# Performance work log

Hardware: AMD Instinct MI355X
Metric: run time of the kernel (lower is better)

The kernel has to match this reference:

```python
import jax, jax.numpy as jnp
import numpy as np

D_MODEL = 1024
NUM_HEADS = 16
HEAD_DIM = D_MODEL // NUM_HEADS
WINDOW = 64
GLOBAL_TOKENS = 4
MAX_SEQ_LEN = 2048
RANDOM_TOKENS = 32
BATCH = 2
SEQ = 2048
NEG = -1.0e9
LN_EPS = 1e-5


def setup_inputs() -> dict:
    key = jax.random.key(0)
    k1, k2, k3, k4 = jax.random.split(key, 4)
    x = jax.random.normal(k1, (BATCH, SEQ, D_MODEL), dtype=jnp.float32)
    w_qkv = jax.random.normal(k2, (D_MODEL, 3 * D_MODEL), dtype=jnp.float32) * (D_MODEL ** -0.5)
    w_out = jax.random.normal(k3, (D_MODEL, D_MODEL), dtype=jnp.float32) * (D_MODEL ** -0.5)
    ln_gamma = jnp.ones((D_MODEL,), dtype=jnp.float32)
    ln_beta = jnp.zeros((D_MODEL,), dtype=jnp.float32)
    rand_idx = jax.random.randint(k4, (MAX_SEQ_LEN, RANDOM_TOKENS), 0, MAX_SEQ_LEN, dtype=jnp.int32)
    return {"x": x, "w_qkv": w_qkv, "w_out": w_out,
            "ln_gamma": ln_gamma, "ln_beta": ln_beta, "rand_idx": rand_idx}


def _build_masks(seq_len, rand_idx):
    i = jnp.arange(seq_len)
    causal = (i[:, None] >= i[None, :]).astype(jnp.float32)  # [L,L], lower-triangular
    # local window mask
    dist = jnp.abs(i[:, None] - i[None, :])
    local = (dist <= WINDOW).astype(jnp.float32) * causal
    # global column mask: columns {0..G-1} u {L-G..L-1}, rows i >= g (== causal on those cols)
    gcols = jnp.concatenate([jnp.arange(GLOBAL_TOKENS), jnp.arange(seq_len - GLOBAL_TOKENS, seq_len)])
    is_gcol = jnp.zeros((seq_len,), jnp.float32).at[gcols].set(1.0)
    glob = is_gcol[None, :] * causal
    # random mask: per-row fixed random columns, then causal-filtered
    ri = rand_idx[:seq_len]  # [L, R]
    rows = jnp.broadcast_to(i[:, None], ri.shape)
    rnd = jnp.zeros((seq_len, seq_len), jnp.float32).at[rows, ri].set(1.0) * causal
    return local, glob, rnd


def reference(x, w_qkv, w_out, ln_gamma, ln_beta, rand_idx):
    B, L, _ = x.shape
    residual = x
    # LayerNorm
    mu = jnp.mean(x, axis=-1, keepdims=True)
    var = jnp.mean(jnp.square(x - mu), axis=-1, keepdims=True)
    xn = (x - mu) * jax.lax.rsqrt(var + LN_EPS) * ln_gamma + ln_beta
    # QKV projection
    qkv = xn @ w_qkv
    q, k, v = jnp.split(qkv, 3, axis=-1)
    q = q.reshape(B, L, NUM_HEADS, HEAD_DIM).transpose(0, 2, 1, 3)  # [B,H,L,D]
    k = k.reshape(B, L, NUM_HEADS, HEAD_DIM).transpose(0, 2, 1, 3)
    v = v.reshape(B, L, NUM_HEADS, HEAD_DIM).transpose(0, 2, 1, 3)
    local, glob, rnd = _build_masks(L, rand_idx)
    raw = jnp.einsum('bhqd,bhkd->bhqk', q, k) / jnp.sqrt(jnp.float32(HEAD_DIM))
    # original sums three masked copies of the same scores:
    # combined = 3*raw + ((1-local)+(1-glob)+(1-rnd)) * NEG
    penalty = (3.0 - (local + glob + rnd)) * NEG  # [L,L]
    combined = 3.0 * raw + penalty[None, None, :, :]
    attn = jax.nn.softmax(combined, axis=-1)
    out = jnp.einsum('bhqk,bhkd->bhqd', attn, v)
    out = out.transpose(0, 2, 1, 3).reshape(B, L, D_MODEL)
    out = out @ w_out
    return out + residual
```

## Files before the change

kernel.cpp:

```cpp
#include <hip/hip_runtime.h>
#include <stdint.h>

typedef __attribute__((ext_vector_type(8))) short shortx8;
typedef __attribute__((ext_vector_type(4))) float floatx4;

static constexpr int SEQ_    = 2048;
static constexpr int DMODEL  = 1024;
static constexpr int HDIM    = 64;
static constexpr int BATCH_  = 2;
static constexpr int NHEADS  = 16;
static constexpr int WINDOW_ = 64;
static constexpr int GTOK    = 4;
static constexpr int RTOK    = 32;
static constexpr int ROWS    = BATCH_ * SEQ_;
static constexpr int QKVN    = 3 * DMODEL;

__device__ inline unsigned short f2bf(float f) {
  union { float f; unsigned int u; } x; x.f = f;
  unsigned int r = (x.u + 0x7FFFu + ((x.u >> 16) & 1u)) >> 16;
  return (unsigned short)r;
}
__device__ inline float bf2f(unsigned short b) {
  union { unsigned int u; float f; } x; x.u = ((unsigned int)b) << 16;
  return x.f;
}

__device__ inline void gload_lds16(const void* g, void* l) {
  __builtin_amdgcn_global_load_lds(
      (const __attribute__((address_space(1))) void*)g,
      (__attribute__((address_space(3))) void*)l, 16, 0, 0);
}

__device__ __forceinline__ void gemm_bk64_128x64(
    const unsigned short* __restrict__ aP0, const unsigned short* __restrict__ aP1,
    const unsigned short* __restrict__ aP2, const unsigned short* __restrict__ aP3,
    const unsigned short* __restrict__ bP0, const unsigned short* __restrict__ bP1,
    unsigned short* smem, const int wave, const int lane, floatx4 (&acc)[4][2]) {
  const int quad = lane >> 4, l16 = lane & 15;
  const int wm = (wave >> 1) * 64, wn = (wave & 1) * 32;
  const int h = l16 & 7;
  auto STAGE = [&](int c, int k0) {
    unsigned short* Ad = smem + c * 12288 + wave * 2048;
    unsigned short* Bd = smem + c * 12288 + 8192 + wave * 1024;
    gload_lds16(aP0 + k0, Ad);
    gload_lds16(aP1 + k0, Ad + 512);
    gload_lds16(aP2 + k0, Ad + 1024);
    gload_lds16(aP3 + k0, Ad + 1536);
    gload_lds16(bP0 + k0, Bd);
    gload_lds16(bP1 + k0, Bd + 512);
  };
  auto COMPUTE = [&](int c) {
    const unsigned short* A = smem + c * 12288;
    const unsigned short* B = A + 8192;
    #pragma unroll
    for (int kk = 0; kk < 2; kk++) {
      shortx8 af[4], bfr[2];
      #pragma unroll
      for (int s = 0; s < 4; s++)
        af[s] = *(const shortx8*)&A[(wm + s * 16 + l16) * 64 + (((quad + kk * 4) ^ h) * 8)];
      #pragma unroll
      for (int s = 0; s < 2; s++)
        bfr[s] = *(const shortx8*)&B[(wn + s * 16 + l16) * 64 + (((quad + kk * 4) ^ h) * 8)];
      #pragma unroll
      for (int sm = 0; sm < 4; sm++)
        #pragma unroll
        for (int sn = 0; sn < 2; sn++)
          acc[sm][sn] = __builtin_amdgcn_mfma_f32_16x16x32_bf16(af[sm], bfr[sn], acc[sm][sn], 0, 0, 0);
    }
  };
  STAGE(0, 0);
  int cur = 0;
  #pragma unroll 1
  for (int t = 0; t < 15; ++t) {
    STAGE(cur ^ 1, (t + 1) * 64);
    asm volatile("s_waitcnt vmcnt(6)" ::: "memory");
    __builtin_amdgcn_s_barrier();
    __builtin_amdgcn_sched_barrier(0);
    COMPUTE(cur);
    __builtin_amdgcn_sched_barrier(0);
    __builtin_amdgcn_s_barrier();
    cur ^= 1;
  }
  asm volatile("s_waitcnt vmcnt(0)" ::: "memory");
  __builtin_amdgcn_s_barrier();
  __builtin_amdgcn_sched_barrier(0);
  COMPUTE(cur);
}

__device__ __forceinline__ void gemm_bk64_64x64_p3(
    const unsigned short* __restrict__ aP0, const unsigned short* __restrict__ aP1,
    const unsigned short* __restrict__ bP0, const unsigned short* __restrict__ bP1,
    unsigned short* smem, const int wave, const int lane, floatx4 (&acc)[2][2]) {
  const int quad = lane >> 4, l16 = lane & 15;
  const int wm = (wave >> 1) * 32, wn = (wave & 1) * 32;
  const int h = l16 & 7;
  auto STAGE = [&](int c, int k0) {
    unsigned short* Ad = smem + c * 8192 + wave * 1024;
    unsigned short* Bd = smem + c * 8192 + 4096 + wave * 1024;
    gload_lds16(aP0 + k0, Ad);
    gload_lds16(aP1 + k0, Ad + 512);
    gload_lds16(bP0 + k0, Bd);
    gload_lds16(bP1 + k0, Bd + 512);
  };
  auto COMPUTE = [&](int c) {
    const unsigned short* A = smem + c * 8192;
    const unsigned short* B = A + 4096;
    #pragma unroll
    for (int kk = 0; kk < 2; kk++) {
      shortx8 af[2], bfr[2];
      #pragma unroll
      for (int s = 0; s < 2; s++)
        af[s] = *(const shortx8*)&A[(wm + s * 16 + l16) * 64 + (((quad + kk * 4) ^ h) * 8)];
      #pragma unroll
      for (int s = 0; s < 2; s++)
        bfr[s] = *(const shortx8*)&B[(wn + s * 16 + l16) * 64 + (((quad + kk * 4) ^ h) * 8)];
      #pragma unroll
      for (int sm = 0; sm < 2; sm++)
        #pragma unroll
        for (int sn = 0; sn < 2; sn++)
          acc[sm][sn] = __builtin_amdgcn_mfma_f32_16x16x32_bf16(af[sm], bfr[sn], acc[sm][sn], 0, 0, 0);
    }
  };
  STAGE(0, 0);
  STAGE(1, 64);
  int cs = 2, cc = 0;
  #pragma unroll 1
  for (int t = 0; t < 14; ++t) {
    STAGE(cs, (t + 2) * 64);
    cs = (cs == 2) ? 0 : cs + 1;
    asm volatile("s_waitcnt vmcnt(8)" ::: "memory");
    __builtin_amdgcn_s_barrier();
    __builtin_amdgcn_sched_barrier(0);
    COMPUTE(cc);
    cc = (cc == 2) ? 0 : cc + 1;
    __builtin_amdgcn_sched_barrier(0);
    __builtin_amdgcn_s_barrier();
  }
  asm volatile("s_waitcnt vmcnt(4)" ::: "memory");
  __builtin_amdgcn_s_barrier();
  __builtin_amdgcn_sched_barrier(0);
  COMPUTE(cc);
  cc = (cc == 2) ? 0 : cc + 1;
  __builtin_amdgcn_sched_barrier(0);
  __builtin_amdgcn_s_barrier();
  asm volatile("s_waitcnt vmcnt(0)" ::: "memory");
  __builtin_amdgcn_s_barrier();
  __builtin_amdgcn_sched_barrier(0);
  COMPUTE(cc);
}

__global__ __launch_bounds__(256) void k1_prep(
    const float* __restrict__ x, const float* __restrict__ w_qkv,
    const float* __restrict__ w_out, const float* __restrict__ gamma,
    const float* __restrict__ beta, const int* __restrict__ ridx,
    unsigned short* __restrict__ xn, unsigned short* __restrict__ wqT,
    unsigned short* __restrict__ woT, unsigned short* __restrict__ Wvs,
    int* __restrict__ cols, int* __restrict__ cnt, int* __restrict__ tmx,
    int* __restrict__ cnts2, int* __restrict__ qlist) {
  __shared__ float tile[64][33];
  __shared__ int rl2[2][RTOK];
  __shared__ int scw2[2], scnw2[2], stm2[2];
  const int bx = blockIdx.x;
  const int t = threadIdx.x;
  if (bx < 1536) {
    const int n0 = (bx % 96) * 32, k0 = (bx / 96) * 64;
    const int tx = t & 31, ty = t >> 5;
    #pragma unroll
    for (int r = ty; r < 64; r += 8)
      tile[r][tx] = w_qkv[(size_t)(k0 + r) * QKVN + n0 + tx];
    __syncthreads();
    #pragma unroll
    for (int r = ty; r < 32; r += 8) {
      unsigned int lo = f2bf(tile[2 * tx][r]);
      unsigned int hi = f2bf(tile[2 * tx + 1][r]);
      *(unsigned int*)&wqT[(size_t)(n0 + r) * DMODEL + k0 + 2 * tx] = lo | (hi << 16);
    }
  } else if (bx < 2560) {
    const int wave = t >> 6, lane = t & 63;
    const int row = (bx - 1536) * 4 + wave;
    const float4* xr = (const float4*)(x + (size_t)row * DMODEL);
    float4 v[4];
    #pragma unroll
    for (int j = 0; j < 4; j++) v[j] = xr[lane + j * 64];
    float s = 0.f;
    #pragma unroll
    for (int j = 0; j < 4; j++) s += v[j].x + v[j].y + v[j].z + v[j].w;
    #pragma unroll
    for (int o = 32; o > 0; o >>= 1) s += __shfl_xor(s, o);
    const float mean = s * (1.0f / DMODEL);
    float q = 0.f;
    #pragma unroll
    for (int j = 0; j < 4; j++) {
      float a = v[j].x - mean, b = v[j].y - mean, c = v[j].z - mean, d = v[j].w - mean;
      q += a * a + b * b + c * c + d * d;
    }
    #pragma unroll
    for (int o = 32; o > 0; o >>= 1) q += __shfl_xor(q, o);
    const float rs = rsqrtf(q * (1.0f / DMODEL) + 1e-5f);
    ushort4* xo = (ushort4*)(xn + (size_t)row * DMODEL);
    #pragma unroll
    for (int j = 0; j < 4; j++) {
      float4 g = ((const float4*)gamma)[lane + j * 64];
      float4 bb = ((const float4*)beta)[lane + j * 64];
      ushort4 ov;
      ov.x = f2bf((v[j].x - mean) * rs * g.x + bb.x);
      ov.y = f2bf((v[j].y - mean) * rs * g.y + bb.y);
      ov.z = f2bf((v[j].z - mean) * rs * g.z + bb.z);
      ov.w = f2bf((v[j].w - mean) * rs * g.w + bb.w);
      xo[lane + j * 64] = ov;
    }
  } else if (bx < 3072) {
    const int idx = bx - 2560;
    const int n0 = (idx & 31) * 32, k0 = (idx >> 5) * 64;
    const int tx = t & 31, ty = t >> 5;
    #pragma unroll
    for (int r = ty; r < 64; r += 8)
      tile[r][tx] = w_out[(size_t)(k0 + r) * DMODEL + n0 + tx];
    __syncthreads();
    #pragma unroll
    for (int r = ty; r < 32; r += 8) {
      unsigned int lo = f2bf(tile[2 * tx][r]);
      unsigned int hi = f2bf(tile[2 * tx + 1][r]);
      *(unsigned int*)&woT[(size_t)(n0 + r) * DMODEL + k0 + 2 * tx] = lo | (hi << 16);
    }
  } else if (bx < 3584) {
    const int idx = bx - 3072;
    const int v0 = (idx & 15) * 64, k0 = (idx >> 4) * 32;
    const int tx = t & 31, ty = t >> 5;
    #pragma unroll
    for (int r = ty; r < 32; r += 8) {
      const float2 w = *(const float2*)&w_qkv[(size_t)(k0 + r) * QKVN + 2 * DMODEL + v0 + 2 * tx];
      unsigned int lo = f2bf(w.x);
      unsigned int hi = f2bf(w.y);
      *(unsigned int*)&Wvs[(size_t)(k0 + r) * DMODEL + v0 + 2 * tx] = lo | (hi << 16);
    }
  } else {
    const int h = t >> 7, c = t & 127;
    const int i = (bx - 3584) * 2 + h;
    if (c < RTOK) rl2[h][c] = ridx[i * RTOK + c];
    if (c == 0) { scw2[h] = 0; scnw2[h] = 0; stm2[h] = 0; }
    __syncthreads();
    const int wstart = (i - WINDOW_ > 0) ? (i - WINDOW_) : 0;
    int j = -1;
    bool valid = false;
    bool iswin = (c < 65);
    if (c < 65) {
      j = i - WINDOW_ + c;
      valid = (j >= 0);
    } else if (c < 73) {
      int g = c - 65;
      j = (g < 4) ? g : (SEQ_ - 8 + g);
      valid = (j <= i) && (j < wstart);
    } else if (c < 73 + RTOK) {
      int r = c - 73;
      j = rl2[h][r];
      bool dup = false;
      for (int r2 = 0; r2 < r; r2++) dup = dup || (rl2[h][r2] == j);
      valid = (j <= i) && (j < wstart) && !(j < GTOK || j >= SEQ_ - GTOK) && !dup;
    }
    int tier = -1;
    if (valid) {
      int loc = ((i - j) <= WINDOW_) ? 1 : 0;
      int glb = (j < GTOK || j >= SEQ_ - GTOK) ? 1 : 0;
      int rnd = 0;
      for (int r = 0; r < RTOK; r++) rnd |= (rl2[h][r] == j) ? 1 : 0;
      tier = loc + glb + rnd;
      atomicMax(&stm2[h], tier);
    }
    __syncthreads();
    const int tm = stm2[h];
    if (valid && tier == tm) {
      if (iswin) {
        int pos = atomicAdd(&scw2[h], 1);
        cols[i * 128 + pos] = j;
      } else {
        int pos = 127 - atomicAdd(&scnw2[h], 1);
        cols[i * 128 + pos] = j;
      }
    }
    __syncthreads();
    if (c == 0) {
      cnt[i] = scw2[h] + scnw2[h];
      tmx[i] = tm;
      cnts2[i] = scw2[h] | (scnw2[h] << 16);
      if (i < 68 || i >= SEQ_ - 4) {
        int cc = (i < 68) ? i : 68 + (i - (SEQ_ - 4));
        qlist[cc * 2 + 0] = (tm == 3) ? i : -1;
        qlist[cc * 2 + 1] = (tm == 3) ? (SEQ_ + i) : -1;
      }
    }
  }
}

__global__ __launch_bounds__(256) void k2_wgemm(
    const unsigned short* __restrict__ woT, const unsigned short* __restrict__ Wvs,
    unsigned short* __restrict__ WvoT, const unsigned short* __restrict__ xn,
    const unsigned short* __restrict__ wqT, const int* __restrict__ qlist,
    unsigned short* __restrict__ qf, unsigned short* __restrict__ kf,
    unsigned short* __restrict__ vf) {
  __shared__ __align__(16) unsigned short smem[2 * 12288];
  const int bx = blockIdx.x, t = threadIdx.x;
  const int wave = t >> 6, lane = t & 63;
  const int quad = lane >> 4, l16 = lane & 15;
  const int wm = (wave >> 1) * 64, wn = (wave & 1) * 32;
  const int r8 = lane >> 3;
  const int swo = ((lane & 7) ^ r8) * 8;
  floatx4 acc[4][2] = {};
  if (bx < 128) {
    const int bm = (bx >> 4) * 128, bn = (bx & 15) * 64;
    const unsigned short* a0 = woT + (size_t)(bm + wave * 32 + r8) * DMODEL + swo;
    const unsigned short* b0 = Wvs + (size_t)(bn + wave * 16 + r8) * DMODEL + swo;
    gemm_bk64_128x64(a0, a0 + 8 * DMODEL, a0 + 16 * DMODEL, a0 + 24 * DMODEL,
                     b0, b0 + 8 * DMODEL, smem, wave, lane, acc);
    #pragma unroll
    for (int sm = 0; sm < 4; sm++)
      #pragma unroll
      for (int sn = 0; sn < 2; sn++)
        #pragma unroll
        for (int r = 0; r < 4; r++) {
          int row = bm + wm + sm * 16 + quad * 4 + r;
          int col = bn + wn + sn * 16 + l16;
          WvoT[(size_t)row * DMODEL + col] = f2bf(acc[sm][sn][r]);
        }
  } else {
    const int idx = bx - 128;
    const int job = idx >> 4, bn = (idx & 15) * 64;
    const int wsel = (job < 2) ? 0 : ((job == 2) ? 1 : 2);
    const unsigned short* BT = wqT + (size_t)wsel * DMODEL * DMODEL;
    unsigned short* dstbuf = (job == 0) ? qf
                           : (job == 1) ? (qf + (size_t)128 * DMODEL)
                           : (job == 2) ? kf : vf;
    const unsigned short* aPg[4];
    #pragma unroll
    for (int g = 0; g < 4; g++) {
      int m = wave * 32 + g * 8 + r8;
      int row;
      if (job < 2) {
        int s = job * 128 + m;
        int ql = (s < 144) ? qlist[s] : -1;
        row = (ql < 0) ? 0 : ql;
      } else {
        row = (m < 16) ? ((m >> 3) * SEQ_ + (((m & 7) < 4) ? (m & 7) : (SEQ_ - 8 + (m & 7)))) : 0;
      }
      aPg[g] = xn + (size_t)row * DMODEL + swo;
    }
    const unsigned short* b0 = BT + (size_t)(bn + wave * 16 + r8) * DMODEL + swo;
    gemm_bk64_128x64(aPg[0], aPg[1], aPg[2], aPg[3],
                     b0, b0 + 8 * DMODEL, smem, wave, lane, acc);
    #pragma unroll
    for (int sm = 0; sm < 4; sm++)
      #pragma unroll
      for (int sn = 0; sn < 2; sn++)
        #pragma unroll
        for (int r = 0; r < 4; r++) {
          int m = wm + sm * 16 + quad * 4 + r;
          int col = bn + wn + sn * 16 + l16;
          dstbuf[(size_t)m * DMODEL + col] = f2bf(acc[sm][sn][r]);
        }
  }
}

__global__ __launch_bounds__(256) void k3_xbar(
    const unsigned short* __restrict__ xn, const int* __restrict__ cols,
    const int* __restrict__ cnt, const int* __restrict__ tmx,
    const int* __restrict__ cnts2, const int* __restrict__ qlist,
    const unsigned short* __restrict__ qf, const unsigned short* __restrict__ kf,
    const unsigned short* __restrict__ vf,
    unsigned short* __restrict__ xbar, unsigned short* __restrict__ vbar) {
  const int bx = blockIdx.x, t = threadIdx.x;
  const int wave = t >> 6, lane = t & 63;
  if (bx >= 36) {
    __shared__ unsigned short win[80][256];
    const int xb = bx - 36;
    const int b = xb >> 9, rest = xb & 511;
    const int i0 = (rest >> 2) * 16, dimbase = (rest & 3) * 256;
    const size_t xnb = (size_t)(b * SEQ_) * DMODEL;
    const int lo = i0 - 64;
    const int r0 = i0 + wave * 4;
    int tm_[4], cw_[4], cnw_[4], jr0_[4], jr1_[4];
    #pragma unroll
    for (int rr = 0; rr < 4; rr++) {
      const int i = r0 + rr;
      tm_[rr] = tmx[i];
      int c2 = cnts2[i];
      cw_[rr] = c2 & 0xffff; cnw_[rr] = c2 >> 16;
      jr0_[rr] = cols[i * 128 + lane];
      jr1_[rr] = cols[i * 128 + 64 + lane];
    }
    {
      const int l5 = lane & 31, rsub = lane >> 5;
      #pragma unroll 5
      for (int it = 0; it < 10; it++) {
        int r = it * 8 + wave * 2 + rsub;
        int gr = lo + r;
        if (gr >= 0)
          *(int4*)&win[r][l5 * 8] =
              *(const int4*)(xn + xnb + (size_t)gr * DMODEL + dimbase + l5 * 8);
      }
    }
    __syncthreads();
    const unsigned short* xnd = xn + xnb + dimbase + lane * 4;
    auto add4 = [](float4& s, ushort4 v) {
      s.x += bf2f(v.x); s.y += bf2f(v.y); s.z += bf2f(v.z); s.w += bf2f(v.w);
    };
    auto sub4 = [](float4& s, ushort4 v) {
      s.x -= bf2f(v.x); s.y -= bf2f(v.y); s.z -= bf2f(v.z); s.w -= bf2f(v.w);
    };
    float4 ws = {0, 0, 0, 0};
    {
      float4 t1 = {0,0,0,0}, t2 = {0,0,0,0}, t3 = {0,0,0,0};
      const int jstart = (r0 - 64 > 0) ? (r0 - 64) : 0;
      const int cn = r0 - jstart + 1;
      const int base = jstart - lo;
      int c = 0;
      for (; c + 4 <= cn; c += 4) {
        ushort4 v0 = *(const ushort4*)&win[base + c][lane * 4];
        ushort4 v1 = *(const ushort4*)&win[base + c + 1][lane * 4];
        ushort4 v2 = *(const ushort4*)&win[base + c + 2][lane * 4];
        ushort4 v3 = *(const ushort4*)&win[base + c + 3][lane * 4];
        add4(ws, v0); add4(t1, v1); add4(t2, v2); add4(t3, v3);
      }
      for (; c < cn; c++) add4(ws, *(const ushort4*)&win[base + c][lane * 4]);
      ws.x += t1.x + t2.x + t3.x; ws.y += t1.y + t2.y + t3.y;
      ws.z += t1.z + t2.z + t3.z; ws.w += t1.w + t2.w + t3.w;
    }
    for (int rr = 0; rr < 4; rr++) {
      const int i = r0 + rr;
      if (rr > 0) {
        add4(ws, *(const ushort4*)&win[i - lo][lane * 4]);
        int dj = i - 65;
        if (dj >= 0) sub4(ws, *(const ushort4*)&win[dj - lo][lane * 4]);
      }
      const int tm = tm_[rr];
      ushort4 o;
      if (tm == 3) {
        o.x = o.y = o.z = o.w = 0;
      } else {
        const int cw = cw_[rr], cnw = cnw_[rr];
        const int jr1 = jr1_[rr];
        float4 s;
        if (tm == 1) {
          s = ws;
          float4 t1 = {0,0,0,0}, t2 = {0,0,0,0}, t3 = {0,0,0,0};
          const int bb = 64 - cnw;
          int c = 0;
          for (; c + 8 <= cnw; c += 8) {
            ushort4 v0 = *(const ushort4*)(xnd + (size_t)__shfl(jr1, bb + c)     * DMODEL);
            ushort4 v1 = *(const ushort4*)(xnd + (size_t)__shfl(jr1, bb + c + 1) * DMODEL);
            ushort4 v2 = *(const ushort4*)(xnd + (size_t)__shfl(jr1, bb + c + 2) * DMODEL);
            ushort4 v3 = *(const ushort4*)(xnd + (size_t)__shfl(jr1, bb + c + 3) * DMODEL);
            ushort4 v4 = *(const ushort4*)(xnd + (size_t)__shfl(jr1, bb + c + 4) * DMODEL);
            ushort4 v5 = *(const ushort4*)(xnd + (size_t)__shfl(jr1, bb + c + 5) * DMODEL);
            ushort4 v6 = *(const ushort4*)(xnd + (size_t)__shfl(jr1, bb + c + 6) * DMODEL);
            ushort4 v7 = *(const ushort4*)(xnd + (size_t)__shfl(jr1, bb + c + 7) * DMODEL);
            add4(s, v0); add4(t1, v1); add4(t2, v2); add4(t3, v3);
            add4(s, v4); add4(t1, v5); add4(t2, v6); add4(t3, v7);
          }
          if (c + 4 <= cnw) {
            ushort4 v0 = *(const ushort4*)(xnd + (size_t)__shfl(jr1, bb + c)     * DMODEL);
            ushort4 v1 = *(const ushort4*)(xnd + (size_t)__shfl(jr1, bb + c + 1) * DMODEL);
            ushort4 v2 = *(const ushort4*)(xnd + (size_t)__shfl(jr1, bb + c + 2) * DMODEL);
            ushort4 v3 = *(const ushort4*)(xnd + (size_t)__shfl(jr1, bb + c + 3) * DMODEL);
            add4(s, v0); add4(t1, v1); add4(t2, v2); add4(t3, v3);
            c += 4;
          }
          for (; c < cnw; c++)
            add4(s, *(const ushort4*)(xnd + (size_t)__shfl(jr1, bb + c) * DMODEL));
          s.x += t1.x + t2.x + t3.x; s.y += t1.y + t2.y + t3.y;
          s.z += t1.z + t2.z + t3.z; s.w += t1.w + t2.w + t3.w;
        } else {
          const int jr0 = jr0_[rr];
          s.x = s.y = s.z = s.w = 0.f;
          for (int c = 0; c < cw; c++) {
            int j = (c < 64) ? __shfl(jr0, c) : __shfl(jr1, c - 64);
            add4(s, *(const ushort4*)(xnd + (size_t)j * DMODEL));
          }
          const int bb = 64 - cnw;
          for (int c = 0; c < cnw; c++)
            add4(s, *(const ushort4*)(xnd + (size_t)__shfl(jr1, bb + c) * DMODEL));
        }
        const float inv = 1.0f / (float)(cw + cnw);
        o.x = f2bf(s.x * inv); o.y = f2bf(s.y * inv);
        o.z = f2bf(s.z * inv); o.w = f2bf(s.w * inv);
      }
      *(ushort4*)(xbar + (size_t)(b * SEQ_ + i) * DMODEL + dimbase + lane * 4) = o;
    }
  } else {
    const int s = bx * 4 + wave;
    const int dst = (s < 144) ? qlist[s] : -1;
    if (dst < 0) return;
    const int b = dst >> 11, i = dst & (SEQ_ - 1);
    const int n = cnt[i];
    int myk = 0;
    if (lane < n) {
      int kj = cols[i * 128 + lane];
      myk = b * 8 + ((kj < 4) ? kj : (kj - (SEQ_ - 8)));
    }
    for (int h = 0; h < NHEADS; h++) {
      float qd = bf2f(qf[(size_t)s * DMODEL + h * HDIM + lane]);
      float w[8];
      float m = -1e30f;
      for (int c = 0; c < n; c++) {
        int ks = __shfl(myk, c);
        float kd = bf2f(kf[(size_t)ks * DMODEL + h * HDIM + lane]);
        float p = qd * kd;
        #pragma unroll
        for (int o = 32; o > 0; o >>= 1) p += __shfl_xor(p, o);
        p *= 0.375f;
        w[c] = p;
        m = fmaxf(m, p);
      }
      float denom = 0.f, acc = 0.f;
      for (int c = 0; c < n; c++) {
        int ks = __shfl(myk, c);
        float e = __expf(w[c] - m);
        denom += e;
        acc += e * bf2f(vf[(size_t)ks * DMODEL + h * HDIM + lane]);
      }
      vbar[(size_t)s * DMODEL + h * HDIM + lane] = f2bf(acc / denom);
    }
  }
}

__global__ __launch_bounds__(256) void k4_final(
    const unsigned short* __restrict__ xbar, const unsigned short* __restrict__ WvoT,
    const unsigned short* __restrict__ vbar, const unsigned short* __restrict__ woT,
    const int* __restrict__ qlist, const int* __restrict__ tmx,
    const float* __restrict__ x, float* __restrict__ out) {
  __shared__ __align__(16) unsigned short smem[3 * 8192];
  __shared__ int rowinf[64];
  const int bx = blockIdx.x, t = threadIdx.x;
  const int wave = t >> 6, lane = t & 63;
  const int quad = lane >> 4, l16 = lane & 15;
  const int wm = (wave >> 1) * 32, wn = (wave & 1) * 32;
  const int r8 = lane >> 3;
  const int swo = ((lane & 7) ^ r8) * 8;
  floatx4 acc[2][2] = {};
  if (bx < 1024) {
    const int bs = (bx & 7) * 128 + (bx >> 3);
    const int bm = (bs >> 4) * 64, bn = (bs & 15) * 64;
    if (t < 64) rowinf[t] = tmx[(bm + t) & (SEQ_ - 1)];
    const unsigned short* a0 = xbar + (size_t)(bm + wave * 16 + r8) * DMODEL + swo;
    const unsigned short* b0 = WvoT + (size_t)(bn + wave * 16 + r8) * DMODEL + swo;
    gemm_bk64_64x64_p3(a0, a0 + 8 * DMODEL, b0, b0 + 8 * DMODEL, smem, wave, lane, acc);
    #pragma unroll
    for (int sm = 0; sm < 2; sm++)
      #pragma unroll
      for (int sn = 0; sn < 2; sn++)
        #pragma unroll
        for (int r = 0; r < 4; r++) {
          int m = wm + sm * 16 + quad * 4 + r;
          if (rowinf[m] != 3) {
            int col = bn + wn + sn * 16 + l16;
            size_t off = (size_t)(bm + m) * DMODEL + col;
            out[off] = acc[sm][sn][r] + x[off];
          }
        }
  } else {
    const int idx = bx - 1024;
    const int bm = (idx >> 4) * 64, bn = (idx & 15) * 64;
    if (t < 64) {
      int s = bm + t;
      rowinf[t] = (s < 144) ? qlist[s] : -1;
    }
    const unsigned short* a0 = vbar + (size_t)(bm + wave * 16 + r8) * DMODEL + swo;
    const unsigned short* b0 = woT + (size_t)(bn + wave * 16 + r8) * DMODEL + swo;
    gemm_bk64_64x64_p3(a0, a0 + 8 * DMODEL, b0, b0 + 8 * DMODEL, smem, wave, lane, acc);
    #pragma unroll
    for (int sm = 0; sm < 2; sm++)
      #pragma unroll
      for (int sn = 0; sn < 2; sn++)
        #pragma unroll
        for (int r = 0; r < 4; r++) {
          int m = wm + sm * 16 + quad * 4 + r;
          int dst = rowinf[m];
          if (dst >= 0) {
            int col = bn + wn + sn * 16 + l16;
            size_t off = (size_t)dst * DMODEL + col;
            out[off] = acc[sm][sn][r] + x[off];
          }
        }
  }
}

extern "C" void kernel_launch(void* const* d_in, const int* in_sizes, int n_in,
                              void* d_out, int out_size, void* d_ws, size_t ws_size,
                              hipStream_t stream) {
  const float* x     = (const float*)d_in[0];
  const float* w_qkv = (const float*)d_in[1];
  const float* w_out = (const float*)d_in[2];
  const float* gamma = (const float*)d_in[3];
  const float* beta  = (const float*)d_in[4];
  const int*   ridx  = (const int*)d_in[5];
  float* out = (float*)d_out;

  char* ws = (char*)d_ws;
  size_t off = 0;
  auto alloc = [&](size_t bytes) {
    char* p = ws + off;
    off = (off + bytes + 255) & ~(size_t)255;
    return p;
  };
  unsigned short* xn   = (unsigned short*)alloc((size_t)ROWS * DMODEL * 2);
  unsigned short* wqT  = (unsigned short*)alloc((size_t)QKVN * DMODEL * 2);
  unsigned short* woT  = (unsigned short*)alloc((size_t)DMODEL * DMODEL * 2);
  unsigned short* Wvs  = (unsigned short*)alloc((size_t)DMODEL * DMODEL * 2);
  unsigned short* WvoT = (unsigned short*)alloc((size_t)DMODEL * DMODEL * 2);
  unsigned short* xbar = (unsigned short*)alloc((size_t)ROWS * DMODEL * 2);
  unsigned short* qf   = (unsigned short*)alloc((size_t)256 * DMODEL * 2);
  unsigned short* kf   = (unsigned short*)alloc((size_t)128 * DMODEL * 2);
  unsigned short* vf   = (unsigned short*)alloc((size_t)128 * DMODEL * 2);
  unsigned short* vbar = (unsigned short*)alloc((size_t)256 * DMODEL * 2);
  int* cols  = (int*)alloc((size_t)SEQ_ * 128 * 4);
  int* cnt   = (int*)alloc((size_t)SEQ_ * 4);
  int* tmx   = (int*)alloc((size_t)SEQ_ * 4);
  int* cnts2 = (int*)alloc((size_t)SEQ_ * 4);
  int* qlist = (int*)alloc(256 * 4);

  hipLaunchKernelGGL(k1_prep, dim3(4608), dim3(256), 0, stream,
                     x, w_qkv, w_out, gamma, beta, ridx,
                     xn, wqT, woT, Wvs, cols, cnt, tmx, cnts2, qlist);
  hipLaunchKernelGGL(k2_wgemm, dim3(192), dim3(256), 0, stream,
                     woT, Wvs, WvoT, xn, wqT, qlist, qf, kf, vf);
  hipLaunchKernelGGL(k3_xbar, dim3(1060), dim3(256), 0, stream,
                     xn, cols, cnt, tmx, cnts2, qlist, qf, kf, vf, xbar, vbar);
  hipLaunchKernelGGL(k4_final, dim3(1072), dim3(256), 0, stream,
                     xbar, WvoT, vbar, woT, qlist, tmx, x, out);
}
```

Measured before the change: 153.9 us.

## Split-K the final output GEMM with atomic accumulation and residual pre-copy

The main output GEMM in k4 is split into two K halves, doubling the block count, and each half accumulates into the output with fp32 atomic adds. The residual x is copied into the output by extra blocks appended to the k2 launch, so k4 no longer reads x. The gathered vbar GEMM also switches to atomic adds. This trades more parallelism and shorter per-block K loops for atomic read-modify-write traffic and an extra full output copy.

New measurement: 165.1 us. 7.2% more time.

```diff
diff --git a/kernel.cpp b/kernel.cpp
--- a/kernel.cpp
+++ b/kernel.cpp
@@ -87,6 +87,7 @@
   COMPUTE(cur);
 }
 
+template<int NT>
 __device__ __forceinline__ void gemm_bk64_64x64_p3(
     const unsigned short* __restrict__ aP0, const unsigned short* __restrict__ aP1,
     const unsigned short* __restrict__ bP0, const unsigned short* __restrict__ bP1,
@@ -125,7 +126,7 @@
   STAGE(1, 64);
   int cs = 2, cc = 0;
   #pragma unroll 1
-  for (int t = 0; t < 14; ++t) {
+  for (int t = 0; t < NT - 2; ++t) {
     STAGE(cs, (t + 2) * 64);
     cs = (cs == 2) ? 0 : cs + 1;
     asm volatile("s_waitcnt vmcnt(8)" ::: "memory");
@@ -297,7 +298,8 @@
     unsigned short* __restrict__ WvoT, const unsigned short* __restrict__ xn,
     const unsigned short* __restrict__ wqT, const int* __restrict__ qlist,
     unsigned short* __restrict__ qf, unsigned short* __restrict__ kf,
-    unsigned short* __restrict__ vf) {
+    unsigned short* __restrict__ vf,
+    const float* __restrict__ x, float* __restrict__ out) {
   __shared__ __align__(16) unsigned short smem[2 * 12288];
   const int bx = blockIdx.x, t = threadIdx.x;
   const int wave = t >> 6, lane = t & 63;
@@ -305,6 +307,16 @@
   const int wm = (wave >> 1) * 64, wn = (wave & 1) * 32;
   const int r8 = lane >> 3;
   const int swo = ((lane & 7) ^ r8) * 8;
+  if (bx >= 192) {
+    const int cb = bx - 192;
+    const float4* xs = (const float4*)x;
+    float4* od = (float4*)out;
+    const int base = cb * 4096;
+    #pragma unroll 4
+    for (int idx = base + t; idx < base + 4096; idx += 256)
+      od[idx] = xs[idx];
+    return;
+  }
   floatx4 acc[4][2] = {};
   if (bx < 128) {
     const int bm = (bx >> 4) * 128, bn = (bx & 15) * 64;
@@ -526,7 +538,7 @@
     const unsigned short* __restrict__ xbar, const unsigned short* __restrict__ WvoT,
     const unsigned short* __restrict__ vbar, const unsigned short* __restrict__ woT,
     const int* __restrict__ qlist, const int* __restrict__ tmx,
-    const float* __restrict__ x, float* __restrict__ out) {
+    float* __restrict__ out) {
   __shared__ __align__(16) unsigned short smem[3 * 8192];
   __shared__ int rowinf[64];
   const int bx = blockIdx.x, t = threadIdx.x;
@@ -536,13 +548,14 @@
   const int r8 = lane >> 3;
   const int swo = ((lane & 7) ^ r8) * 8;
   floatx4 acc[2][2] = {};
-  if (bx < 1024) {
-    const int bs = (bx & 7) * 128 + (bx >> 3);
+  if (bx < 2048) {
+    const int b = bx & 1023, kh = bx >> 10;
+    const int bs = (b & 7) * 128 + (b >> 3);
     const int bm = (bs >> 4) * 64, bn = (bs & 15) * 64;
     if (t < 64) rowinf[t] = tmx[(bm + t) & (SEQ_ - 1)];
-    const unsigned short* a0 = xbar + (size_t)(bm + wave * 16 + r8) * DMODEL + swo;
-    const unsigned short* b0 = WvoT + (size_t)(bn + wave * 16 + r8) * DMODEL + swo;
-    gemm_bk64_64x64_p3(a0, a0 + 8 * DMODEL, b0, b0 + 8 * DMODEL, smem, wave, lane, acc);
+    const unsigned short* a0 = xbar + (size_t)(bm + wave * 16 + r8) * DMODEL + kh * 512 + swo;
+    const unsigned short* b0 = WvoT + (size_t)(bn + wave * 16 + r8) * DMODEL + kh * 512 + swo;
+    gemm_bk64_64x64_p3<8>(a0, a0 + 8 * DMODEL, b0, b0 + 8 * DMODEL, smem, wave, lane, acc);
     #pragma unroll
     for (int sm = 0; sm < 2; sm++)
       #pragma unroll
@@ -552,12 +565,11 @@
           int m = wm + sm * 16 + quad * 4 + r;
           if (rowinf[m] != 3) {
             int col = bn + wn + sn * 16 + l16;
-            size_t off = (size_t)(bm + m) * DMODEL + col;
-            out[off] = acc[sm][sn][r] + x[off];
+            unsafeAtomicAdd(&out[(size_t)(bm + m) * DMODEL + col], acc[sm][sn][r]);
           }
         }
   } else {
-    const int idx = bx - 1024;
+    const int idx = bx - 2048;
     const int bm = (idx >> 4) * 64, bn = (idx & 15) * 64;
     if (t < 64) {
       int s = bm + t;
@@ -565,7 +577,7 @@
     }
     const unsigned short* a0 = vbar + (size_t)(bm + wave * 16 + r8) * DMODEL + swo;
     const unsigned short* b0 = woT + (size_t)(bn + wave * 16 + r8) * DMODEL + swo;
-    gemm_bk64_64x64_p3(a0, a0 + 8 * DMODEL, b0, b0 + 8 * DMODEL, smem, wave, lane, acc);
+    gemm_bk64_64x64_p3<16>(a0, a0 + 8 * DMODEL, b0, b0 + 8 * DMODEL, smem, wave, lane, acc);
     #pragma unroll
     for (int sm = 0; sm < 2; sm++)
       #pragma unroll
@@ -576,8 +588,7 @@
           int dst = rowinf[m];
           if (dst >= 0) {
             int col = bn + wn + sn * 16 + l16;
-            size_t off = (size_t)dst * DMODEL + col;
-            out[off] = acc[sm][sn][r] + x[off];
+            unsafeAtomicAdd(&out[(size_t)dst * DMODEL + col], acc[sm][sn][r]);
           }
         }
   }
@@ -620,10 +631,10 @@
   hipLaunchKernelGGL(k1_prep, dim3(4608), dim3(256), 0, stream,
                      x, w_qkv, w_out, gamma, beta, ridx,
                      xn, wqT, woT, Wvs, cols, cnt, tmx, cnts2, qlist);
-  hipLaunchKernelGGL(k2_wgemm, dim3(192), dim3(256), 0, stream,
-                     woT, Wvs, WvoT, xn, wqT, qlist, qf, kf, vf);
+  hipLaunchKernelGGL(k2_wgemm, dim3(448), dim3(256), 0, stream,
+                     woT, Wvs, WvoT, xn, wqT, qlist, qf, kf, vf, x, out);
   hipLaunchKernelGGL(k3_xbar, dim3(1060), dim3(256), 0, stream,
                      xn, cols, cnt, tmx, cnts2, qlist, qf, kf, vf, xbar, vbar);
-  hipLaunchKernelGGL(k4_final, dim3(1072), dim3(256), 0, stream,
-                     xbar, WvoT, vbar, woT, qlist, tmx, x, out);
-}
+  hipLaunchKernelGGL(k4_final, dim3(2096), dim3(256), 0, stream,
+                     xbar, WvoT, vbar, woT, qlist, tmx, out);
+}
```
